# Kernel tuning notes

Measured on AMD Instinct MI355X. Metric: run time of the kernel, lower is better.

Reference implementation:

```python
import jax, jax.numpy as jnp
from jax import lax
import numpy as np

# larq-style ste_sign: forward sign (with sign(0)=+1), straight-through grad clipped to |x|<=1
@jax.custom_vjp
def ste_sign(x):
    return jnp.where(x >= 0, 1.0, -1.0).astype(x.dtype)

def _ste_fwd(x):
    return ste_sign(x), x

def _ste_bwd(x, g):
    return (g * (jnp.abs(x) <= 1.0).astype(g.dtype),)

ste_sign.defvjp(_ste_fwd, _ste_bwd)


def setup_inputs() -> dict:
    key = jax.random.key(0)
    k1, k2 = jax.random.split(key)
    B, H, Wd, Cin = 16, 256, 256, 32
    M, kh, kw, Cout = 4, 3, 3, 32
    x = jax.random.normal(k1, (B, H, Wd, Cin), dtype=jnp.float32)
    W = jax.random.normal(k2, (M, kh, kw, Cin, Cout), dtype=jnp.float32)
    b = jnp.zeros((M, Cout), dtype=jnp.float32)
    return {"x": x, "W": W, "b": b}


def reference(x, W, b):
    # Multibin: sum_{m} QuantConv2D_m(x).  Each branch binarizes the SAME input,
    # so sum of convs == one conv with the sum of the binarized kernels (fused).
    xq = ste_sign(x)                 # [B,H,W,Cin], values in {-1,+1}
    wq = ste_sign(W)                 # [M,kh,kw,Cin,Cout]
    w_sum = wq.sum(axis=0)           # [kh,kw,Cin,Cout]
    y = lax.conv_general_dilated(
        xq, w_sum,
        window_strides=(1, 1),
        padding="SAME",
        dimension_numbers=("NHWC", "HWIO", "NHWC"),
    )
    return y + b.sum(axis=0)         # [B,H,W,Cout]
```

## Files before the change

### kernel.cpp

```cpp
#include <hip/hip_runtime.h>


#define RH      8
#define PITCHB  48
#define PSLOT   (34 * PITCHB)
#define RSLOT   4096
#define RAWOFF  (4 * PSLOT)
#define SLOTP   2048
#define NRING   5
#define XQOFF   16384
#define XQSZ    50331648
#define WSNEED  (XQOFF + XQSZ + 4096)

typedef __attribute__((ext_vector_type(4)))  int i32x4;
typedef __attribute__((ext_vector_type(16))) int i32x16;

__device__ __forceinline__ void gload16(const void* g, void* l) {
    __builtin_amdgcn_global_load_lds(
        (const __attribute__((address_space(1))) void*)g,
        (__attribute__((address_space(3))) void*)l, 16, 0, 0);
}

__device__ __forceinline__ unsigned packsgn4(uint4 v) {
    unsigned r;
    r  =  (__uint_as_float(v.x) >= 0.0f) ? 0x01u : 0xFFu;
    r |= ((__uint_as_float(v.y) >= 0.0f) ? 0x01u : 0xFFu) << 8;
    r |= ((__uint_as_float(v.z) >= 0.0f) ? 0x01u : 0xFFu) << 16;
    r |= ((__uint_as_float(v.w) >= 0.0f) ? 0x01u : 0xFFu) << 24;
    return r;
}

__device__ __forceinline__ unsigned packsgn4f(float4 v) {
    unsigned r;
    r  =  ((v.x >= 0.0f) ? 0x01u : 0xFFu);
    r |= ((v.y >= 0.0f) ? 0x01u : 0xFFu) << 8;
    r |= ((v.z >= 0.0f) ? 0x01u : 0xFFu) << 16;
    r |= ((v.w >= 0.0f) ? 0x01u : 0xFFu) << 24;
    return r;
}

__global__ void prep_kernel(const float* __restrict__ W, const float* __restrict__ bias,
                            signed char* __restrict__ wsT, float* __restrict__ bsum) {
    int t = blockIdx.x * 256 + threadIdx.x;
    if (t < 9216) {
        int k   = t >> 5;
        int co  = t & 31;
        int tap = k >> 5;
        int ci  = k & 31;
        float s = 0.0f;
        #pragma unroll
        for (int m = 0; m < 4; ++m) {
            float w = W[(m * 9 + tap) * 1024 + ci * 32 + co];
            s += (w >= 0.0f) ? 1.0f : -1.0f;
        }
        wsT[co * 288 + k] = (signed char)(int)s;
    }
    if (t < 32) {
        float s = 0.0f;
        #pragma unroll
        for (int m = 0; m < 4; ++m) s += bias[m * 32 + t];
        bsum[t] = s;
    }
}

__global__ __launch_bounds__(256) void pack_kernel(const float* __restrict__ x,
                                                   unsigned char* __restrict__ xq) {
    int t = blockIdx.x * 256 + threadIdx.x;
    #pragma unroll
    for (int it = 0; it < 4; ++it) {
        int idx = t + it * 2097152;
        float4 v = ((const float4*)x)[idx];
        unsigned r = packsgn4f(v);
        int px = idx >> 3, u = idx & 7;
        *(unsigned*)(xq + (long)px * 48 + u * 4) = r;
    }
}

#define WAITV(N)                                                                \
    do {                                                                        \
        asm volatile("s_waitcnt vmcnt(" #N ")" ::: "memory");                   \
        __builtin_amdgcn_sched_barrier(0);                                      \
    } while (0)

#define ISSUE_P(J)                                                              \
    do {                                                                        \
        const int row_  = r0 - 1 + (J);                                         \
        const int rowc_ = row_ < 0 ? 0 : (row_ > 255 ? 255 : row_);             \
        const char* gb_ = (const char*)xq +                                     \
            ((long)(bimg * 256 + rowc_) * 256 + (c0 - 1)) * 48;                 \
        unsigned char* lb_ = lds + ((J) % NRING) * SLOTP;                       \
        gload16(gb_ + lane * 16, lb_);                                          \
        gload16(gb_ + 1024 + lane * 16, lb_ + 1024);                            \
        __builtin_amdgcn_sched_barrier(0);                                      \
    } while (0)

#define COMMIT_P(J)                                                             \
    do {                                                                        \
        const int row_   = r0 - 1 + (J);                                        \
        const bool rowok_ = (row_ >= 0) && (row_ < 256);                        \
        unsigned char* sl_ = lds + ((J) % NRING) * SLOTP;                       \
        if (!rowok_) {                                                          \
            if (lane < 34) {                                                    \
                *(uint4*)(sl_ + lane * 48)      = zr4;                          \
                *(uint4*)(sl_ + lane * 48 + 16) = zr4;                          \
            }                                                                   \
        } else if (hz_on) {                                                     \
            *(uint4*)(sl_ + hz_ad) = zr4;                                       \
        }                                                                       \
    } while (0)

__global__ __launch_bounds__(64, 4) void conv_packed(const unsigned char* __restrict__ xq,
                                                     const signed char* __restrict__ wsT,
                                                     const float* __restrict__ bsum,
                                                     float* __restrict__ out) {
    __shared__ __align__(16) unsigned char lds[NRING * SLOTP];

    const int lane = threadIdx.x;
    const int lrow = lane & 31;
    const int lk   = lane >> 5;

    const int bs   = blockIdx.x;
    const int c0   = (bs & 7) * 32;
    const int r0   = ((bs >> 3) & 31) * RH;
    const int bimg = bs >> 8;

    i32x4 bfrag[9];
    #pragma unroll
    for (int t = 0; t < 9; ++t)
        bfrag[t] = *(const i32x4*)(wsT + lrow * 288 + t * 32 + lk * 16);
    const float bsv = bsum[lrow];

    const uint4 zr4 = make_uint4(0u, 0u, 0u, 0u);
    const bool hz_on = ((c0 == 0) && (lane < 2)) ||
                       ((c0 == 224) && (lane >= 2) && (lane < 4));
    const int  hz_ad = (lane < 2) ? lane * 16 : (33 * 48 + (lane - 2) * 16);

    ISSUE_P(0);
    ISSUE_P(1);
    ISSUE_P(2);
    WAITV(4);  COMMIT_P(0);
    WAITV(2);  COMMIT_P(1);
    ISSUE_P(3);
    WAITV(2);  COMMIT_P(2);

    const int a_base = lrow * 48 + lk * 16;

    #pragma unroll
    for (int i = 0; i < RH; ++i) {
        if (i <= RH - 3) ISSUE_P(i + 4);

        if (i == 0)      { WAITV(2);  }
        else if (i <= 5) { WAITV(18); }
        else if (i == 6) { WAITV(16); }
        if (i <= RH - 2) COMMIT_P(i + 3);

        i32x16 acc = {};
        #pragma unroll
        for (int dh = 0; dh < 3; ++dh) {
            const unsigned char* sb = lds + ((i + dh) % NRING) * SLOTP;
            #pragma unroll
            for (int dw = 0; dw < 3; ++dw) {
                i32x4 a = *(const i32x4*)(sb + a_base + dw * 48);
                acc = __builtin_amdgcn_mfma_i32_32x32x32_i8(a, bfrag[dh * 3 + dw],
                                                            acc, 0, 0, 0);
            }
        }

        float* op = out + ((long)((bimg * 256 + (r0 + i)) * 256 + c0)) * 32 + lrow;
        #pragma unroll
        for (int reg = 0; reg < 16; ++reg) {
            int pr = (reg & 3) + 8 * (reg >> 2) + 4 * lk;
            op[pr * 32] = (float)acc[reg] + bsv;
        }
    }
}

#define HSEL(J) ((((J) % 3) == 0) ? h0 : ((((J) % 3) == 1) ? h1 : h2))

#define ISSUE_ROW(J, HREG)                                                      \
    do {                                                                        \
        const int row_  = r0 - 1 + (J);                                         \
        const int rowc_ = row_ < 0 ? 0 : (row_ > 255 ? 255 : row_);             \
        const char* gb_ = (const char*)(x + (long)((bimg * 256 + rowc_) * 256   \
                                                   + c0) * 32);                 \
        unsigned char* lb_ = lds + RAWOFF + ((J) % 3) * RSLOT;                  \
        _Pragma("unroll")                                                       \
        for (int k_ = 0; k_ < 4; ++k_)                                          \
            gload16(gb_ + k_ * 1024 + lswz16, lb_ + k_ * 1024);                 \
        HREG = *(x + (long)(bimg * 256 + rowc_) * 8192 + hoff);                 \
        __builtin_amdgcn_sched_barrier(0);                                      \
    } while (0)

#define PACK_ROW(J, HREG)                                                       \
    do {                                                                        \
        const int row_   = r0 - 1 + (J);                                        \
        const bool rowok_ = (row_ >= 0) && (row_ < 256);                        \
        unsigned char* ps_ = lds + ((J) & 3) * PSLOT;                           \
        const unsigned char* rs_ = lds + RAWOFF + ((J) % 3) * RSLOT;            \
        ps_[hpx * PITCHB + (lane & 31)] =                                       \
            (rowok_ && hok) ? ((HREG >= 0.0f) ? 0x01 : 0xFF) : 0;               \
        uint4 o_;                                                               \
        if (rowok_) {                                                           \
            uint4 w0_ = *(const uint4*)(rs_ + (ppx * 8 + ((ph * 4 + 0) ^ pxr)) * 16); \
            uint4 w1_ = *(const uint4*)(rs_ + (ppx * 8 + ((ph * 4 + 1) ^ pxr)) * 16); \
            uint4 w2_ = *(const uint4*)(rs_ + (ppx * 8 + ((ph * 4 + 2) ^ pxr)) * 16); \
            uint4 w3_ = *(const uint4*)(rs_ + (ppx * 8 + ((ph * 4 + 3) ^ pxr)) * 16); \
            o_ = make_uint4(packsgn4(w0_), packsgn4(w1_),                       \
                            packsgn4(w2_), packsgn4(w3_));                      \
        } else {                                                                \
            o_ = make_uint4(0u, 0u, 0u, 0u);                                    \
        }                                                                       \
        *(uint4*)(ps_ + (ppx + 1) * PITCHB + ph * 16) = o_;                     \
    } while (0)

__global__ __launch_bounds__(64, 2) void conv_fused(const float* __restrict__ x,
                                                    const signed char* __restrict__ wsT,
                                                    const float* __restrict__ bsum,
                                                    float* __restrict__ out) {
    __shared__ __align__(16) unsigned char lds[4 * PSLOT + 3 * RSLOT];

    const int lane = threadIdx.x;
    const int lrow = lane & 31;
    const int lk   = lane >> 5;

    const int bs   = blockIdx.x;
    const int c0   = (bs & 7) * 32;
    const int r0   = ((bs >> 3) & 31) * RH;
    const int bimg = bs >> 8;

    i32x4 bfrag[9];
    #pragma unroll
    for (int t = 0; t < 9; ++t)
        bfrag[t] = *(const i32x4*)(wsT + lrow * 288 + t * 32 + lk * 16);
    const float bsv = bsum[lrow];

    const int lswz16 = (lane ^ ((lane >> 3) & 7)) * 16;
    const int hcol   = (lane < 32) ? (c0 > 0 ? c0 - 1 : 0)
                                   : (c0 + 32 < 256 ? c0 + 32 : 255);
    const bool hok   = (lane < 32) ? (c0 > 0) : (c0 + 32 < 256);
    const int  hpx   = (lane < 32) ? 0 : 33;
    const long hoff  = (long)hcol * 32 + (lane & 31);
    const int  ppx   = lane >> 1;
    const int  ph    = lane & 1;
    const int  pxr   = ppx & 7;

    float h0 = 0.f, h1 = 0.f, h2 = 0.f;

    ISSUE_ROW(0, HSEL(0));
    ISSUE_ROW(1, HSEL(1));
    ISSUE_ROW(2, HSEL(2));
    WAITV(10);  PACK_ROW(0, HSEL(0));
    WAITV(5);   PACK_ROW(1, HSEL(1));
    ISSUE_ROW(3, HSEL(3));
    WAITV(5);   PACK_ROW(2, HSEL(2));

    const int a_off = lrow * PITCHB + lk * 16;

    #pragma unroll
    for (int i = 0; i < RH; ++i) {
        if (i <= RH - 3) ISSUE_ROW(i + 4, HSEL(i + 4));

        if (i == 0)      { WAITV(5);  }
        else if (i <= 5) { WAITV(21); }
        else if (i == 6) { WAITV(16); }
        if (i <= RH - 2) PACK_ROW(i + 3, HSEL(i + 3));

        i32x16 acc = {};
        #pragma unroll
        for (int dh = 0; dh < 3; ++dh) {
            const unsigned char* sb = lds + ((i + dh) & 3) * PSLOT + a_off;
            #pragma unroll
            for (int dw = 0; dw < 3; ++dw) {
                i32x4 a = *(const i32x4*)(sb + dw * PITCHB);
                acc = __builtin_amdgcn_mfma_i32_32x32x32_i8(a, bfrag[dh * 3 + dw],
                                                            acc, 0, 0, 0);
            }
        }

        float* op = out + ((long)((bimg * 256 + (r0 + i)) * 256 + c0)) * 32 + lrow;
        #pragma unroll
        for (int reg = 0; reg < 16; ++reg) {
            int pr = (reg & 3) + 8 * (reg >> 2) + 4 * lk;
            op[pr * 32] = (float)acc[reg] + bsv;
        }
    }
}

extern "C" void kernel_launch(void* const* d_in, const int* in_sizes, int n_in,
                              void* d_out, int out_size, void* d_ws, size_t ws_size,
                              hipStream_t stream) {
    const float* x    = (const float*)d_in[0];
    const float* W    = (const float*)d_in[1];
    const float* bias = (const float*)d_in[2];
    float* out = (float*)d_out;

    signed char* wsT  = (signed char*)d_ws;
    float* bsum       = (float*)((char*)d_ws + 9216);
    unsigned char* xq = (unsigned char*)d_ws + XQOFF;

    prep_kernel<<<36, 256, 0, stream>>>(W, bias, wsT, bsum);
    if (ws_size >= (size_t)WSNEED) {
        pack_kernel<<<8192, 256, 0, stream>>>(x, xq);
        conv_packed<<<4096, 64, 0, stream>>>(xq, wsT, bsum, out);
    } else {
        conv_fused<<<4096, 64, 0, stream>>>(x, wsT, bsum, out);
    }
}
```

Baseline: 270.1 us.

## Load all input rows upfront in conv kernel and widen pack kernel stores

The conv kernel drops its 5-slot ring buffer with staged waits. It now issues global-to-LDS loads for all 10 needed rows at once, waits a single time, applies the zero padding, then runs the MFMA loop without further synchronisation. This removes the per-row wait and commit overhead, but uses twice the LDS and lowers the occupancy hint from 4 to 2. The pack kernel now has each thread handle half a pixel with 16-byte stores and zero-fill the padding bytes, replacing the 4-byte strided stores.

```diff
diff --git a/kernel.cpp b/kernel.cpp
--- a/kernel.cpp
+++ b/kernel.cpp
@@ -6,8 +6,8 @@
 #define PSLOT   (34 * PITCHB)
 #define RSLOT   4096
 #define RAWOFF  (4 * PSLOT)
-#define SLOTP   2048
-#define NRING   5
+#define SLOTB2  2048
+#define NSLOT   10
 #define XQOFF   16384
 #define XQSZ    50331648
 #define WSNEED  (XQOFF + XQSZ + 4096)
@@ -65,15 +65,17 @@
 
 __global__ __launch_bounds__(256) void pack_kernel(const float* __restrict__ x,
                                                    unsigned char* __restrict__ xq) {
-    int t = blockIdx.x * 256 + threadIdx.x;
-    #pragma unroll
-    for (int it = 0; it < 4; ++it) {
-        int idx = t + it * 2097152;
-        float4 v = ((const float4*)x)[idx];
-        unsigned r = packsgn4f(v);
-        int px = idx >> 3, u = idx & 7;
-        *(unsigned*)(xq + (long)px * 48 + u * 4) = r;
-    }
+    int t  = blockIdx.x * 256 + threadIdx.x;
+    int px = t >> 1, h = t & 1;
+    const char* src = (const char*)x + (long)px * 128 + h * 64;
+    uint4 v0 = *(const uint4*)(src);
+    uint4 v1 = *(const uint4*)(src + 16);
+    uint4 v2 = *(const uint4*)(src + 32);
+    uint4 v3 = *(const uint4*)(src + 48);
+    uint4 sg = make_uint4(packsgn4(v0), packsgn4(v1), packsgn4(v2), packsgn4(v3));
+    unsigned char* dst = xq + (long)px * 48 + h * 16;
+    *(uint4*)dst = sg;
+    if (h) *(uint4*)(dst + 16) = make_uint4(0u, 0u, 0u, 0u);
 }
 
 #define WAITV(N)                                                                \
@@ -82,38 +84,11 @@
         __builtin_amdgcn_sched_barrier(0);                                      \
     } while (0)
 
-#define ISSUE_P(J)                                                              \
-    do {                                                                        \
-        const int row_  = r0 - 1 + (J);                                         \
-        const int rowc_ = row_ < 0 ? 0 : (row_ > 255 ? 255 : row_);             \
-        const char* gb_ = (const char*)xq +                                     \
-            ((long)(bimg * 256 + rowc_) * 256 + (c0 - 1)) * 48;                 \
-        unsigned char* lb_ = lds + ((J) % NRING) * SLOTP;                       \
-        gload16(gb_ + lane * 16, lb_);                                          \
-        gload16(gb_ + 1024 + lane * 16, lb_ + 1024);                            \
-        __builtin_amdgcn_sched_barrier(0);                                      \
-    } while (0)
-
-#define COMMIT_P(J)                                                             \
-    do {                                                                        \
-        const int row_   = r0 - 1 + (J);                                        \
-        const bool rowok_ = (row_ >= 0) && (row_ < 256);                        \
-        unsigned char* sl_ = lds + ((J) % NRING) * SLOTP;                       \
-        if (!rowok_) {                                                          \
-            if (lane < 34) {                                                    \
-                *(uint4*)(sl_ + lane * 48)      = zr4;                          \
-                *(uint4*)(sl_ + lane * 48 + 16) = zr4;                          \
-            }                                                                   \
-        } else if (hz_on) {                                                     \
-            *(uint4*)(sl_ + hz_ad) = zr4;                                       \
-        }                                                                       \
-    } while (0)
-
-__global__ __launch_bounds__(64, 4) void conv_packed(const unsigned char* __restrict__ xq,
-                                                     const signed char* __restrict__ wsT,
-                                                     const float* __restrict__ bsum,
-                                                     float* __restrict__ out) {
-    __shared__ __align__(16) unsigned char lds[NRING * SLOTP];
+__global__ __launch_bounds__(64, 2) void conv_batch(const unsigned char* __restrict__ xq,
+                                                    const signed char* __restrict__ wsT,
+                                                    const float* __restrict__ bsum,
+                                                    float* __restrict__ out) {
+    __shared__ __align__(16) unsigned char lds[NSLOT * SLOTB2];
 
     const int lane = threadIdx.x;
     const int lrow = lane & 31;
@@ -124,40 +99,51 @@
     const int r0   = ((bs >> 3) & 31) * RH;
     const int bimg = bs >> 8;
 
+    #pragma unroll
+    for (int j = 0; j < NSLOT; ++j) {
+        const int row  = r0 - 1 + j;
+        const int rowc = row < 0 ? 0 : (row > 255 ? 255 : row);
+        const char* gb = (const char*)xq +
+            ((long)(bimg * 256 + rowc) * 256 + (c0 - 1)) * 48;
+        unsigned char* lb = lds + j * SLOTB2;
+        gload16(gb + lane * 16, lb);
+        gload16(gb + 1024 + lane * 16, lb + 1024);
+    }
+
     i32x4 bfrag[9];
     #pragma unroll
     for (int t = 0; t < 9; ++t)
         bfrag[t] = *(const i32x4*)(wsT + lrow * 288 + t * 32 + lk * 16);
     const float bsv = bsum[lrow];
 
+    WAITV(0);
+
     const uint4 zr4 = make_uint4(0u, 0u, 0u, 0u);
-    const bool hz_on = ((c0 == 0) && (lane < 2)) ||
-                       ((c0 == 224) && (lane >= 2) && (lane < 4));
-    const int  hz_ad = (lane < 2) ? lane * 16 : (33 * 48 + (lane - 2) * 16);
-
-    ISSUE_P(0);
-    ISSUE_P(1);
-    ISSUE_P(2);
-    WAITV(4);  COMMIT_P(0);
-    WAITV(2);  COMMIT_P(1);
-    ISSUE_P(3);
-    WAITV(2);  COMMIT_P(2);
+    #pragma unroll
+    for (int j = 0; j < NSLOT; ++j) {
+        const int row = r0 - 1 + j;
+        unsigned char* sl = lds + j * SLOTB2;
+        if (row < 0 || row > 255) {
+            if (lane < 34) {
+                *(uint4*)(sl + lane * 48)      = zr4;
+                *(uint4*)(sl + lane * 48 + 16) = zr4;
+            }
+        } else {
+            if ((c0 == 0) && (lane < 2))
+                *(uint4*)(sl + lane * 16) = zr4;
+            if ((c0 == 224) && (lane >= 2) && (lane < 4))
+                *(uint4*)(sl + 33 * 48 + (lane - 2) * 16) = zr4;
+        }
+    }
 
     const int a_base = lrow * 48 + lk * 16;
 
     #pragma unroll
     for (int i = 0; i < RH; ++i) {
-        if (i <= RH - 3) ISSUE_P(i + 4);
-
-        if (i == 0)      { WAITV(2);  }
-        else if (i <= 5) { WAITV(18); }
-        else if (i == 6) { WAITV(16); }
-        if (i <= RH - 2) COMMIT_P(i + 3);
-
         i32x16 acc = {};
         #pragma unroll
         for (int dh = 0; dh < 3; ++dh) {
-            const unsigned char* sb = lds + ((i + dh) % NRING) * SLOTP;
+            const unsigned char* sb = lds + (i + dh) * SLOTB2;
             #pragma unroll
             for (int dw = 0; dw < 3; ++dw) {
                 i32x4 a = *(const i32x4*)(sb + a_base + dw * 48);
@@ -165,7 +151,6 @@
                                                             acc, 0, 0, 0);
             }
         }
-
         float* op = out + ((long)((bimg * 256 + (r0 + i)) * 256 + c0)) * 32 + lrow;
         #pragma unroll
         for (int reg = 0; reg < 16; ++reg) {
@@ -301,7 +286,7 @@
     prep_kernel<<<36, 256, 0, stream>>>(W, bias, wsT, bsum);
     if (ws_size >= (size_t)WSNEED) {
         pack_kernel<<<8192, 256, 0, stream>>>(x, xq);
-        conv_packed<<<4096, 64, 0, stream>>>(xq, wsT, bsum, out);
+        conv_batch<<<4096, 64, 0, stream>>>(xq, wsT, bsum, out);
     } else {
         conv_fused<<<4096, 64, 0, stream>>>(x, wsT, bsum, out);
     }
```

Result: faster. 257.6 us (-4.6%).
